# Kernel optimization log

Hardware: AMD Instinct MI355X
Metric: run time of the kernel (lower is better)

The kernel has to match this reference:

```python
import jax, jax.numpy as jnp
import numpy as np

K = 6  # hardcoded top-k in the original forward


def setup_inputs() -> dict:
    key = jax.random.key(0)
    k1, k2, k3, k4, k5 = jax.random.split(key, 5)
    N, M, C = 512, 2048, 256
    return {
        "micro": jax.random.normal(k1, (N, C), jnp.float32),
        "label": jax.random.uniform(k2, (N,), jnp.float32),
        "micro_all": jax.random.normal(k3, (M, C), jnp.float32),
        "label_all": jax.random.uniform(k4, (M,), jnp.float32),
        # fc = nn.Linear(channels, 1, bias=False) -> weight vector [C]
        "fc_w": jax.random.normal(k5, (C,), jnp.float32) * 0.05,
    }


def reference(micro, label, micro_all, label_all, fc_w):
    N, C = micro.shape
    M = micro_all.shape[0]
    # Pairwise squared differences: dis[n, m, c] = (micro_all[m,c] - micro[n,c])^2
    dis = (micro_all[None, :, :] - micro[:, None, :]) ** 2  # [N, M, C]
    # Linear(C,1,bias=False) along channel dim, minus per-pair channel mean
    anti = jnp.einsum('nmc,c->nm', dis, fc_w) - dis.mean(axis=2)  # [N, M]
    anti = jax.nn.softmax(anti, axis=1)
    # top-k mask (argsort-based selection of k largest == lax.top_k)
    _, idx = jax.lax.top_k(anti, K)  # [N, K]
    mask = jnp.zeros((N, M), anti.dtype).at[jnp.arange(N)[:, None], idx].set(1.0)
    cut = anti * mask
    cut = cut / jnp.sum(cut, axis=1, keepdims=True)  # renormalize kNN weights
    micro_tmp = micro + cut @ micro_all  # [N, C]
    # composition loss
    dis_label = jnp.abs(label_all[None, :] - label[:, None])  # [N, M]
    co_loss = jnp.asarray(1e-4, cut.dtype) + jnp.sum(dis_label * cut) / N
    return micro_tmp, co_loss
```

## Files before the change

### kernel.cpp

```cpp
#include <hip/hip_runtime.h>
#include <hip/hip_bf16.h>
#include <math.h>

#define N_Q   512
#define M_ALL 2048
#define CHN   256
#define TOPK  6
#define INV_C (1.0f / 256.0f)

#define WS_LOSS  64
#define WS_LOGIT 4096

typedef __bf16 bf16x8 __attribute__((ext_vector_type(8)));
typedef float  f32x4  __attribute__((ext_vector_type(4)));

static __device__ __forceinline__ unsigned short bfbits(float x) {
    __bf16 h = (__bf16)x;
    unsigned short u;
    __builtin_memcpy(&u, &h, 2);
    return u;
}

#define BM 64
#define BN 32
#define LDK 264

__global__ __launch_bounds__(256) void gcn_gemm(
    const float* __restrict__ micro_all,
    const float* __restrict__ micro,
    const float* __restrict__ fc_w,
    float* __restrict__ logits)
{
    __shared__ unsigned short sA[BM][LDK];
    __shared__ unsigned short sB[BN][LDK];
    __shared__ float s_bias[BM];

    const int t    = threadIdx.x;
    const int w    = t >> 6;
    const int l15  = t & 15;
    const int quad = (t >> 4) & 3;
    const int m0   = blockIdx.x * BM;
    const int n0   = blockIdx.y * BN;

    const int rg = t >> 4;
    const int c0 = (t & 15) * 4;

    float4 wv[4];
    #pragma unroll
    for (int cc = 0; cc < 4; ++cc) {
        float4 x = *(const float4*)(fc_w + c0 + cc * 64);
        x.x -= INV_C; x.y -= INV_C; x.z -= INV_C; x.w -= INV_C;
        wv[cc] = x;
    }

    #pragma unroll
    for (int i = 0; i < 4; ++i) {
        const int r = i * 16 + rg;
        const float* rp = micro_all + (size_t)(m0 + r) * CHN;
        float p = 0.0f;
        #pragma unroll
        for (int cc = 0; cc < 4; ++cc) {
            const float4 v = *(const float4*)(rp + c0 + cc * 64);
            const float sx = v.x * wv[cc].x;
            const float sy = v.y * wv[cc].y;
            const float sz = v.z * wv[cc].z;
            const float sw = v.w * wv[cc].w;
            ushort4 pk;
            pk.x = bfbits(sx); pk.y = bfbits(sy); pk.z = bfbits(sz); pk.w = bfbits(sw);
            *(ushort4*)&sA[r][c0 + cc * 64] = pk;
            p += v.x * sx + v.y * sy + v.z * sz + v.w * sw;
        }
        #pragma unroll
        for (int mask = 8; mask >= 1; mask >>= 1)
            p += __shfl_xor(p, mask, 64);
        if ((t & 15) == 0) s_bias[r] = p;
    }

    #pragma unroll
    for (int i = 0; i < 2; ++i) {
        const int r = i * 16 + rg;
        const float* rp = micro + (size_t)(n0 + r) * CHN;
        #pragma unroll
        for (int cc = 0; cc < 4; ++cc) {
            const float4 v = *(const float4*)(rp + c0 + cc * 64);
            ushort4 pk;
            pk.x = bfbits(v.x); pk.y = bfbits(v.y); pk.z = bfbits(v.z); pk.w = bfbits(v.w);
            *(ushort4*)&sB[r][c0 + cc * 64] = pk;
        }
    }
    __syncthreads();

    const int nt    = w & 1;
    const int mtp   = w >> 1;
    const int rowB  = nt * 16 + l15;
    const int rowA0 = mtp * 32 + l15;
    const int rowA1 = mtp * 32 + 16 + l15;

    f32x4 acc0 = {0.f, 0.f, 0.f, 0.f};
    f32x4 acc1 = {0.f, 0.f, 0.f, 0.f};
    #pragma unroll
    for (int ks = 0; ks < 8; ++ks) {
        const int k0 = ks * 32 + quad * 8;
        const bf16x8 a  = *(const bf16x8*)&sB[rowB][k0];
        const bf16x8 b0 = *(const bf16x8*)&sA[rowA0][k0];
        const bf16x8 b1 = *(const bf16x8*)&sA[rowA1][k0];
        acc0 = __builtin_amdgcn_mfma_f32_16x16x32_bf16(a, b0, acc0, 0, 0, 0);
        acc1 = __builtin_amdgcn_mfma_f32_16x16x32_bf16(a, b1, acc1, 0, 0, 0);
    }

    const float bias0 = s_bias[mtp * 32 + l15];
    const float bias1 = s_bias[mtp * 32 + 16 + l15];
    #pragma unroll
    for (int reg = 0; reg < 4; ++reg) {
        const int n = n0 + nt * 16 + quad * 4 + reg;
        logits[(size_t)n * M_ALL + m0 + mtp * 32 + l15]      = bias0 - 2.f * acc0[reg];
        logits[(size_t)n * M_ALL + m0 + mtp * 32 + 16 + l15] = bias1 - 2.f * acc1[reg];
    }
}

#define BLOCK 256
#define WAVES (BLOCK / 64)
#define MPT   (M_ALL / BLOCK)
#define WTOP  8
#define NCAND (WAVES * WTOP)
#define NREF  10

static __device__ __forceinline__ unsigned key_of(float f, int m) {
    unsigned u = __float_as_uint(f);
    u = (u & 0x80000000u) ? ~u : (u | 0x80000000u);
    return (u & 0xFFFFF800u) | (unsigned)m;
}

__global__ __launch_bounds__(BLOCK) void gcn_topk(
    const float* __restrict__ logits,
    const float* __restrict__ micro,
    const float* __restrict__ label,
    const float* __restrict__ micro_all,
    const float* __restrict__ label_all,
    const float* __restrict__ fc_w,
    float* __restrict__ out,
    float* __restrict__ loss_arr)
{
    __shared__ unsigned s_keys[NCAND];
    __shared__ unsigned s_top[NREF];
    __shared__ float    s_ex[NREF];

    const int n    = blockIdx.x;
    const int t    = threadIdx.x;
    const int wave = t >> 6;
    const int lane = t & 63;

    const float4 b4 = *(const float4*)(micro + (size_t)n * CHN + lane * 4);
    float4 w4 = *(const float4*)(fc_w + lane * 4);
    w4.x -= INV_C; w4.y -= INV_C; w4.z -= INV_C; w4.w -= INV_C;

    unsigned k8[MPT];
    #pragma unroll
    for (int j = 0; j < MPT; ++j) {
        const int m = t + j * BLOCK;
        k8[j] = key_of(logits[(size_t)n * M_ALL + m], m);
    }

    #pragma unroll
    for (int k = 0; k < WTOP; ++k) {
        unsigned best = k8[0];
        #pragma unroll
        for (int j = 1; j < MPT; ++j) best = (k8[j] > best) ? k8[j] : best;
        #pragma unroll
        for (int mask = 32; mask > 0; mask >>= 1) {
            const unsigned ov = __shfl_xor(best, mask, 64);
            best = (ov > best) ? ov : best;
        }
        if (lane == 0) s_keys[wave * WTOP + k] = best;
        #pragma unroll
        for (int j = 0; j < MPT; ++j)
            k8[j] = (k8[j] == best) ? 0u : k8[j];
    }
    __syncthreads();

    {
        unsigned v = s_keys[lane & 31];
        #pragma unroll
        for (int k = 2; k <= 32; k <<= 1) {
            #pragma unroll
            for (int j = k >> 1; j >= 1; j >>= 1) {
                const unsigned pv = __shfl_xor(v, j, 64);
                const unsigned mx = (v > pv) ? v : pv;
                const unsigned mn = (v > pv) ? pv : v;
                const bool up    = ((lane & k) == 0);
                const bool lower = ((lane & j) == 0);
                v = (up == lower) ? mx : mn;
            }
        }
        if (wave == 0 && lane < NREF) s_top[lane] = v;
    }
    __syncthreads();

    for (int c = wave; c < NREF; c += WAVES) {
        const int m = (int)(s_top[c] & 0x7FFu);
        const float4 a = *(const float4*)(micro_all + (size_t)m * CHN + lane * 4);
        const float dx = a.x - b4.x;
        const float dy = a.y - b4.y;
        const float dz = a.z - b4.z;
        const float dw = a.w - b4.w;
        float acc = dx * dx * w4.x + dy * dy * w4.y + dz * dz * w4.z + dw * dw * w4.w;
        #pragma unroll
        for (int mask = 32; mask >= 1; mask >>= 1)
            acc += __shfl_xor(acc, mask, 64);
        if (lane == 0) s_ex[c] = acc;
    }
    __syncthreads();

    float top_val[TOPK];
    int   top_idx[TOPK];
    unsigned rtk = 0u;
    #pragma unroll
    for (int k = 0; k < TOPK; ++k) {
        float best = -INFINITY;
        int   bi   = 0;
        #pragma unroll
        for (int c = 0; c < NREF; ++c) {
            const bool avail = ((rtk >> c) & 1u) == 0u;
            const float cv = s_ex[c];
            if (avail && cv > best) { best = cv; bi = c; }
        }
        top_val[k] = best;
        top_idx[k] = (int)(s_top[bi] & 0x7FFu);
        rtk |= 1u << bi;
    }

    const float mx = top_val[0];
    float e[TOPK];
    float esum = 0.0f;
    #pragma unroll
    for (int k = 0; k < TOPK; ++k) { e[k] = __expf(top_val[k] - mx); esum += e[k]; }
    const float inv = 1.0f / esum;

    float outv = micro[(size_t)n * CHN + t];
    #pragma unroll
    for (int k = 0; k < TOPK; ++k)
        outv += (e[k] * inv) * micro_all[(size_t)top_idx[k] * CHN + t];
    out[n * CHN + t] = outv;

    if (t == 0) {
        const float lab = label[n];
        float l = 0.0f;
        #pragma unroll
        for (int k = 0; k < TOPK; ++k)
            l += (e[k] * inv) * fabsf(label_all[top_idx[k]] - lab);
        loss_arr[n] = l;
    }
}

__global__ __launch_bounds__(256) void gcn_finalize(
    const float* __restrict__ loss_arr,
    float* __restrict__ out)
{
    __shared__ float red[4];
    const int t = threadIdx.x;
    float v = loss_arr[t] + loss_arr[t + 256];
    #pragma unroll
    for (int mask = 32; mask >= 1; mask >>= 1)
        v += __shfl_xor(v, mask, 64);
    if ((t & 63) == 0) red[t >> 6] = v;
    __syncthreads();
    if (t == 0)
        out[N_Q * CHN] = 1e-4f + (red[0] + red[1] + red[2] + red[3]) / (float)N_Q;
}

extern "C" void kernel_launch(void* const* d_in, const int* in_sizes, int n_in,
                              void* d_out, int out_size, void* d_ws, size_t ws_size,
                              hipStream_t stream) {
    const float* micro     = (const float*)d_in[0];
    const float* label     = (const float*)d_in[1];
    const float* micro_all = (const float*)d_in[2];
    const float* label_all = (const float*)d_in[3];
    const float* fc_w      = (const float*)d_in[4];
    float* out    = (float*)d_out;
    float* ws     = (float*)d_ws;
    float* loss   = ws + WS_LOSS;
    float* logits = ws + WS_LOGIT;

    gcn_gemm<<<dim3(M_ALL / BM, N_Q / BN), 256, 0, stream>>>(
        micro_all, micro, fc_w, logits);
    gcn_topk<<<N_Q, BLOCK, 0, stream>>>(logits, micro, label, micro_all,
                                        label_all, fc_w, out, loss);
    gcn_finalize<<<1, 256, 0, stream>>>(loss, out);
}
```

Measured before the change: 78.56 us.

## Drop finalize kernel via atomic loss, widen GEMM tile, vectorize logit loads

Removes the third kernel launch by having each top-k block atomically add its scaled loss contribution into the output scalar, which the GEMM kernel initializes to the constant. The GEMM block grows to 64x64 with 512 threads, halving the grid and reducing redundant A-tile staging. Top-k logit loads become contiguous float4 reads per thread, changing which candidates each thread owns. Atomic float accumulation makes the loss order-nondeterministic, and initialization depends on the GEMM kernel running before top-k on the same stream.

Result: slower. 80.94 us (+3.0%).

```diff
diff --git a/kernel.cpp b/kernel.cpp
--- a/kernel.cpp
+++ b/kernel.cpp
@@ -8,7 +8,6 @@
 #define TOPK  6
 #define INV_C (1.0f / 256.0f)
 
-#define WS_LOSS  64
 #define WS_LOGIT 4096
 
 typedef __bf16 bf16x8 __attribute__((ext_vector_type(8)));
@@ -22,14 +21,15 @@
 }
 
 #define BM 64
-#define BN 32
+#define BN 64
 #define LDK 264
 
-__global__ __launch_bounds__(256) void gcn_gemm(
+__global__ __launch_bounds__(512) void gcn_gemm(
     const float* __restrict__ micro_all,
     const float* __restrict__ micro,
     const float* __restrict__ fc_w,
-    float* __restrict__ logits)
+    float* __restrict__ logits,
+    float* __restrict__ out)
 {
     __shared__ unsigned short sA[BM][LDK];
     __shared__ unsigned short sB[BN][LDK];
@@ -42,6 +42,8 @@
     const int m0   = blockIdx.x * BM;
     const int n0   = blockIdx.y * BN;
 
+    if (m0 == 0 && n0 == 0 && t == 0) out[N_Q * CHN] = 1e-4f;
+
     const int rg = t >> 4;
     const int c0 = (t & 15) * 4;
 
@@ -54,8 +56,8 @@
     }
 
     #pragma unroll
-    for (int i = 0; i < 4; ++i) {
-        const int r = i * 16 + rg;
+    for (int i = 0; i < 2; ++i) {
+        const int r = i * 32 + rg;
         const float* rp = micro_all + (size_t)(m0 + r) * CHN;
         float p = 0.0f;
         #pragma unroll
@@ -78,7 +80,7 @@
 
     #pragma unroll
     for (int i = 0; i < 2; ++i) {
-        const int r = i * 16 + rg;
+        const int r = i * 32 + rg;
         const float* rp = micro + (size_t)(n0 + r) * CHN;
         #pragma unroll
         for (int cc = 0; cc < 4; ++cc) {
@@ -90,8 +92,8 @@
     }
     __syncthreads();
 
-    const int nt    = w & 1;
-    const int mtp   = w >> 1;
+    const int nt    = w & 3;
+    const int mtp   = w >> 2;
     const int rowB  = nt * 16 + l15;
     const int rowA0 = mtp * 32 + l15;
     const int rowA1 = mtp * 32 + 16 + l15;
@@ -138,8 +140,7 @@
     const float* __restrict__ micro_all,
     const float* __restrict__ label_all,
     const float* __restrict__ fc_w,
-    float* __restrict__ out,
-    float* __restrict__ loss_arr)
+    float* __restrict__ out)
 {
     __shared__ unsigned s_keys[NCAND];
     __shared__ unsigned s_top[NREF];
@@ -155,10 +156,18 @@
     w4.x -= INV_C; w4.y -= INV_C; w4.z -= INV_C; w4.w -= INV_C;
 
     unsigned k8[MPT];
-    #pragma unroll
-    for (int j = 0; j < MPT; ++j) {
-        const int m = t + j * BLOCK;
-        k8[j] = key_of(logits[(size_t)n * M_ALL + m], m);
+    {
+        const float4 v0 = *(const float4*)(logits + (size_t)n * M_ALL + t * 8);
+        const float4 v1 = *(const float4*)(logits + (size_t)n * M_ALL + t * 8 + 4);
+        const int mb = t * 8;
+        k8[0] = key_of(v0.x, mb + 0);
+        k8[1] = key_of(v0.y, mb + 1);
+        k8[2] = key_of(v0.z, mb + 2);
+        k8[3] = key_of(v0.w, mb + 3);
+        k8[4] = key_of(v1.x, mb + 4);
+        k8[5] = key_of(v1.y, mb + 5);
+        k8[6] = key_of(v1.z, mb + 6);
+        k8[7] = key_of(v1.w, mb + 7);
     }
 
     #pragma unroll
@@ -248,24 +257,8 @@
         #pragma unroll
         for (int k = 0; k < TOPK; ++k)
             l += (e[k] * inv) * fabsf(label_all[top_idx[k]] - lab);
-        loss_arr[n] = l;
-    }
-}
-
-__global__ __launch_bounds__(256) void gcn_finalize(
-    const float* __restrict__ loss_arr,
-    float* __restrict__ out)
-{
-    __shared__ float red[4];
-    const int t = threadIdx.x;
-    float v = loss_arr[t] + loss_arr[t + 256];
-    #pragma unroll
-    for (int mask = 32; mask >= 1; mask >>= 1)
-        v += __shfl_xor(v, mask, 64);
-    if ((t & 63) == 0) red[t >> 6] = v;
-    __syncthreads();
-    if (t == 0)
-        out[N_Q * CHN] = 1e-4f + (red[0] + red[1] + red[2] + red[3]) / (float)N_Q;
+        atomicAdd(out + N_Q * CHN, l * (1.0f / (float)N_Q));
+    }
 }
 
 extern "C" void kernel_launch(void* const* d_in, const int* in_sizes, int n_in,
@@ -278,12 +271,10 @@
     const float* fc_w      = (const float*)d_in[4];
     float* out    = (float*)d_out;
     float* ws     = (float*)d_ws;
-    float* loss   = ws + WS_LOSS;
     float* logits = ws + WS_LOGIT;
 
-    gcn_gemm<<<dim3(M_ALL / BM, N_Q / BN), 256, 0, stream>>>(
-        micro_all, micro, fc_w, logits);
+    gcn_gemm<<<dim3(M_ALL / BM, N_Q / BN), 512, 0, stream>>>(
+        micro_all, micro, fc_w, logits, out);
     gcn_topk<<<N_Q, BLOCK, 0, stream>>>(logits, micro, label, micro_all,
-                                        label_all, fc_w, out, loss);
-    gcn_finalize<<<1, 256, 0, stream>>>(loss, out);
-}
+                                        label_all, fc_w, out);
+}
```
